# Optimization experiments

Hardware: AMD Instinct MI355X
Metric: run time of the kernel (lower is better)

The kernel has to match this reference:

```python
import jax, jax.numpy as jnp
import numpy as np

DIM = 1024
HEADS = 16
DIM_HEAD = 64
INNER = HEADS * DIM_HEAD  # 1024
SCALE = DIM_HEAD ** -0.5


def setup_inputs() -> dict:
    key = jax.random.key(0)
    ks = jax.random.split(key, 5)
    B, N = 4, 2048
    x = jax.random.normal(ks[0], (B, N, DIM), dtype=jnp.float32)
    # torch Linear weights are [out, in]; store transposed [in, out] for x @ W
    s = 1.0 / np.sqrt(DIM)
    Wq = jax.random.uniform(ks[1], (DIM, INNER), minval=-s, maxval=s, dtype=jnp.float32)
    Wkv = jax.random.uniform(ks[2], (DIM, 2 * INNER), minval=-s, maxval=s, dtype=jnp.float32)
    so = 1.0 / np.sqrt(INNER)
    Wo = jax.random.uniform(ks[3], (INNER, DIM), minval=-so, maxval=so, dtype=jnp.float32)
    bo = jax.random.uniform(ks[4], (DIM,), minval=-so, maxval=so, dtype=jnp.float32)
    return {"x": x, "Wq": Wq, "Wkv": Wkv, "Wo": Wo, "bo": bo}


def reference(x, Wq, Wkv, Wo, bo):
    B, N, _ = x.shape
    q = x @ Wq                      # [B, N, INNER]
    kv = x @ Wkv                    # [B, N, 2*INNER]
    k, v = jnp.split(kv, 2, axis=-1)

    def split_heads(t):
        return t.reshape(B, N, HEADS, DIM_HEAD).transpose(0, 2, 1, 3)  # [B,H,N,D]

    q, k, v = split_heads(q) * SCALE, split_heads(k), split_heads(v)
    sim = jnp.einsum('bhid,bhjd->bhij', q, k)  # [B,H,N,N]
    mask_value = -jnp.finfo(sim.dtype).max
    # causal: mask strictly-upper triangle (triu with offset j-i+1 = 1)
    causal_mask = jnp.triu(jnp.ones((N, N), dtype=bool), k=1)
    sim = jnp.where(causal_mask[None, None, :, :], mask_value, sim)
    attn = jax.nn.softmax(sim, axis=-1)
    out = jnp.einsum('bhij,bhjd->bhid', attn, v)            # [B,H,N,D]
    out = out.transpose(0, 2, 1, 3).reshape(B, N, INNER)    # [B,N,INNER]
    return out @ Wo + bo
```

## Files before the change

kernel.cpp:

```cpp
#include <hip/hip_runtime.h>

typedef unsigned short u16;
typedef __bf16 bf16x8 __attribute__((ext_vector_type(8)));
typedef float floatx4 __attribute__((ext_vector_type(4)));
typedef unsigned as1_u32 __attribute__((address_space(1)));
typedef unsigned as3_u32 __attribute__((address_space(3)));

__device__ inline u16 f2bf(float f) {
    unsigned int u = __builtin_bit_cast(unsigned int, f);
    u += 0x7fffu + ((u >> 16) & 1u);
    return (u16)(u >> 16);
}
__device__ inline floatx4 mfma16(bf16x8 a, bf16x8 b, floatx4 c) {
    return __builtin_amdgcn_mfma_f32_16x16x32_bf16(a, b, c, 0, 0, 0);
}
__device__ inline void gld16(const u16* g, u16* l) {
    __builtin_amdgcn_global_load_lds((const as1_u32*)g, (as3_u32*)l, 16, 0, 0);
}
__device__ inline unsigned permpack(float lo, float hi) {
    return __builtin_amdgcn_perm(__builtin_bit_cast(unsigned, hi),
                                 __builtin_bit_cast(unsigned, lo), 0x07060302u);
}

#define NSEQ 2048
#define DIM  1024
#define HEADS 16
#define DHEAD 64
#define QSCALE 0.18033688f
#define CSHIFT 4.328085f

__device__ inline void transpose_tile(const float* __restrict__ src,
                                      u16* __restrict__ dst, int ncols,
                                      int n0, int k0, int t) {
    __shared__ u16 tile[64][72];
    #pragma unroll
    for (int rr = 0; rr < 4; rr++) {
        const int k = (t >> 4) + rr * 16;
        const int n = (t & 15) * 4;
        float4 v = *(const float4*)&src[(size_t)(k0 + k) * ncols + n0 + n];
        tile[n + 0][k] = f2bf(v.x); tile[n + 1][k] = f2bf(v.y);
        tile[n + 2][k] = f2bf(v.z); tile[n + 3][k] = f2bf(v.w);
    }
    __syncthreads();
    #pragma unroll
    for (int ww = 0; ww < 2; ww++) {
        const int idx = t + ww * 256;
        const int n = idx >> 3, g = idx & 7;
        u16 tmp[8] __attribute__((aligned(16)));
        #pragma unroll
        for (int i = 0; i < 8; i++) tmp[i] = tile[n][g * 8 + i];
        *(uint4*)&dst[(size_t)(n0 + n) * 1024 + k0 + g * 8] = *(const uint4*)tmp;
    }
}

__global__ __launch_bounds__(256) void prep_fused(
    const float* __restrict__ x,  u16* __restrict__ xb,
    const float* __restrict__ Wq, const float* __restrict__ Wkv,
    u16* __restrict__ Wt)
{
    const int bid = blockIdx.x;
    const int t = threadIdx.x;
    if (bid < 4096) {
        const size_t i = ((size_t)bid * 256 + t) * 8;
        float4 a = *(const float4*)&x[i];
        float4 b = *(const float4*)&x[i + 4];
        u16 o[8] __attribute__((aligned(16)));
        o[0] = f2bf(a.x); o[1] = f2bf(a.y); o[2] = f2bf(a.z); o[3] = f2bf(a.w);
        o[4] = f2bf(b.x); o[5] = f2bf(b.y); o[6] = f2bf(b.z); o[7] = f2bf(b.w);
        *(uint4*)&xb[i] = *(const uint4*)o;
    } else if (bid < 4352) {
        const int v = bid - 4096;
        transpose_tile(Wq, Wt, 1024, (v & 15) * 64, (v >> 4) * 64, t);
    } else {
        const int v = bid - 4352;
        transpose_tile(Wkv, Wt + (size_t)1024 * 1024, 2048, (v & 31) * 64, (v >> 5) * 64, t);
    }
}

__global__ __launch_bounds__(256) void transpose_conv(const float* __restrict__ src,
                                                      u16* __restrict__ dst, int ncols) {
    transpose_tile(src, dst, ncols, blockIdx.x * 64, blockIdx.y * 64, threadIdx.x);
}

__global__ __launch_bounds__(256) void qkv_gemm_v6(
    const u16* __restrict__ xb, const u16* __restrict__ Wt,
    u16* __restrict__ q_ws, u16* __restrict__ k_ws, u16* __restrict__ v_ws)
{
    __shared__ u16 As[2][2][128 * 32];
    __shared__ u16 Bs[2][2][128 * 32];

    const int n0 = blockIdx.x * 128;
    const int m0 = blockIdx.y * 128;
    const int t = threadIdx.x, lane = t & 63, w = t >> 6;
    const int wr = w >> 1, wc = w & 1;
    const int quad = lane >> 4, l16 = lane & 15;
    const int lrow = lane >> 2;
    const int lk = (((lane & 3) ^ ((lane >> 3) & 3)) * 8);
    const int rsw = ((l16 >> 1) & 3);

    floatx4 acc[4][4];
    #pragma unroll
    for (int i = 0; i < 4; i++)
        #pragma unroll
        for (int j = 0; j < 4; j++) acc[i][j] = floatx4{0.f, 0.f, 0.f, 0.f};

#define STAGE_V6(kt, buf) do {                                             \
    const size_t k0s = (size_t)(kt) * 64;                                  \
    _Pragma("unroll")                                                      \
    for (int hh = 0; hh < 2; hh++) {                                       \
        const int row = w * 32 + hh * 16;                                  \
        const size_t ga = (size_t)(m0 + row + lrow) * DIM + k0s + lk;      \
        const size_t gb = (size_t)(n0 + row + lrow) * DIM + k0s + lk;      \
        gld16(&xb[ga],      &As[buf][0][row * 32]);                        \
        gld16(&xb[ga + 32], &As[buf][1][row * 32]);                        \
        gld16(&Wt[gb],      &Bs[buf][0][row * 32]);                        \
        gld16(&Wt[gb + 32], &Bs[buf][1][row * 32]);                        \
    }                                                                      \
} while (0)

    STAGE_V6(0, 0);
    STAGE_V6(1, 1);

    for (int kt = 0; kt < 16; kt++) {
        const int cur = kt & 1;
        if (kt < 15) asm volatile("s_waitcnt vmcnt(8)" ::: "memory");
        else         asm volatile("s_waitcnt vmcnt(0)" ::: "memory");
        __builtin_amdgcn_s_barrier();
        __builtin_amdgcn_sched_barrier(0);

        #pragma unroll
        for (int ks = 0; ks < 2; ks++) {
            const u16* al = &As[cur][ks][0];
            const u16* bl = &Bs[cur][ks][0];
            bf16x8 af[4], bf[4];
            #pragma unroll
            for (int i = 0; i < 4; i++)
                af[i] = *(const bf16x8*)&al[(wr * 64 + i * 16 + l16) * 32
                                            + ((quad ^ rsw) * 8)];
            #pragma unroll
            for (int j = 0; j < 4; j++)
                bf[j] = *(const bf16x8*)&bl[(wc * 64 + j * 16 + l16) * 32
                                            + ((quad ^ rsw) * 8)];
            __builtin_amdgcn_s_setprio(1);
            #pragma unroll
            for (int i = 0; i < 4; i++)
                #pragma unroll
                for (int j = 0; j < 4; j++)
                    acc[i][j] = mfma16(af[i], bf[j], acc[i][j]);
            __builtin_amdgcn_s_setprio(0);
        }

        __builtin_amdgcn_sched_barrier(0);
        __builtin_amdgcn_s_barrier();
        __builtin_amdgcn_sched_barrier(0);
        if (kt < 14) STAGE_V6(kt + 2, cur);
    }
#undef STAGE_V6

    const int seg = n0 >> 10;
    #pragma unroll
    for (int j = 0; j < 4; j++) {
        const int n  = n0 + wc * 64 + j * 16 + l16;
        const int nn = n & 1023;
        const int h  = nn >> 6, d = nn & 63;
        #pragma unroll
        for (int i = 0; i < 4; i++) {
            const int mb = m0 + wr * 64 + i * 16 + quad * 4;
            const int b = mb >> 11, ib = mb & (NSEQ - 1);
            if (seg == 0) {
                #pragma unroll
                for (int r = 0; r < 4; r++)
                    q_ws[(((size_t)(b * HEADS + h)) * NSEQ + ib + r) * DHEAD + d] =
                        f2bf(acc[i][j][r] * QSCALE);
            } else if (seg == 1) {
                #pragma unroll
                for (int r = 0; r < 4; r++)
                    k_ws[(((size_t)(b * HEADS + h)) * NSEQ + ib + r) * DHEAD + d] =
                        f2bf(acc[i][j][r]);
            } else {
                u16 tmp[4] __attribute__((aligned(8)));
                #pragma unroll
                for (int r = 0; r < 4; r++) tmp[r] = f2bf(acc[i][j][r]);
                *(uint2*)&v_ws[(((size_t)(b * HEADS + h)) * DHEAD + d) * NSEQ + ib] =
                    *(const uint2*)tmp;
            }
        }
    }
}

__global__ __launch_bounds__(256) void attn_v8(
    const u16* __restrict__ q_ws, const u16* __restrict__ k_ws,
    const u16* __restrict__ v_ws, u16* __restrict__ attn_ws)
{
    __shared__ u16 kds[2][64 * 64];
    __shared__ u16 vds[2][64 * 64];
    __shared__ u16 p_lds[4 * 2048];

    const int bid = blockIdx.x;
    const int bh  = bid & 63;
    const int t16 = 15 - (bid >> 6);
    const int i0  = t16 * 128;
    const int b   = bh >> 4, h = bh & 15;

    const u16* qb = q_ws + (size_t)bh * NSEQ * DHEAD;
    const u16* kb = k_ws + (size_t)bh * NSEQ * DHEAD;
    const u16* vb = v_ws + (size_t)bh * DHEAD * NSEQ;

    const int t    = threadIdx.x;
    const int lane = t & 63, w = t >> 6;
    const int quad = lane >> 4, l16 = lane & 15;

    const int srow8 = lane >> 3;
    const int chunk = (lane & 7) ^ srow8;
    const int krow  = w * 16 + srow8;
    const size_t koff = (size_t)krow * DHEAD + chunk * 8;
    const size_t voff = (size_t)krow * NSEQ + chunk * 8;
    u16* klbase = (u16*)&kds[0][0] + w * 1024;
    u16* vlbase = (u16*)&vds[0][0] + w * 1024;
    const int sw = (l16 & 7);

    bf16x8 qf[2][2];
    #pragma unroll
    for (int rf = 0; rf < 2; rf++)
        #pragma unroll
        for (int dg = 0; dg < 2; dg++)
            qf[rf][dg] = *(const bf16x8*)&qb[(size_t)(i0 + rf * 64 + w * 16 + l16) * DHEAD
                                             + dg * 32 + quad * 8];

    floatx4 l4[2] = {floatx4{0.f,0.f,0.f,0.f}, floatx4{0.f,0.f,0.f,0.f}};
    floatx4 acc[2][4];
    #pragma unroll
    for (int rf = 0; rf < 2; rf++)
        #pragma unroll
        for (int dg = 0; dg < 4; dg++) acc[rf][dg] = floatx4{0.f, 0.f, 0.f, 0.f};

    const int jt_max = 2 * t16 + 1;

    gld16(&kb[koff],             klbase);
    gld16(&kb[koff + 8 * DHEAD], klbase + 512);
    gld16(&vb[voff],             vlbase);
    gld16(&vb[voff + 8 * NSEQ],  vlbase + 512);

    for (int jt = 0; jt <= jt_max; jt++) {
        const int cur = jt & 1;
        __syncthreads();

        if (jt < jt_max) {
            const size_t j64 = (size_t)(jt + 1) * 64;
            const int nb = (cur ^ 1) * 4096;
            gld16(&kb[j64 * DHEAD + koff],             klbase + nb);
            gld16(&kb[j64 * DHEAD + koff + 8 * DHEAD], klbase + nb + 512);
            gld16(&vb[j64 + voff],                     vlbase + nb);
            gld16(&vb[j64 + voff + 8 * NSEQ],          vlbase + nb + 512);
        }

        const u16* kl = &kds[cur][0];
        const u16* vl = &vds[cur][0];
        const int j0 = jt * 64;

        floatx4 s[2][4];
        #pragma unroll
        for (int rf = 0; rf < 2; rf++)
            #pragma unroll
            for (int g = 0; g < 4; g++)
                s[rf][g] = floatx4{-CSHIFT, -CSHIFT, -CSHIFT, -CSHIFT};
        __builtin_amdgcn_s_setprio(1);
        #pragma unroll
        for (int dg = 0; dg < 2; dg++)
            #pragma unroll
            for (int g = 0; g < 4; g++) {
                bf16x8 kf = *(const bf16x8*)&kl[(g * 16 + l16) * 64
                                                + (((dg * 4 + quad) ^ sw) * 8)];
                s[0][g] = mfma16(kf, qf[0][dg], s[0][g]);
                s[1][g] = mfma16(kf, qf[1][dg], s[1][g]);
            }
        __builtin_amdgcn_s_setprio(0);

        #pragma unroll
        for (int rf = 0; rf < 2; rf++) {
            const int imin = i0 + rf * 64 + w * 16;
            if (j0 + 63 > imin) {
                const int i = imin + l16;
                #pragma unroll
                for (int g = 0; g < 4; g++) {
                    const int jb = j0 + g * 16 + quad * 4;
                    #pragma unroll
                    for (int r = 0; r < 4; r++)
                        if (jb + r > i) s[rf][g][r] = -1e30f;
                }
            }
        }

        #pragma unroll
        for (int rf = 0; rf < 2; rf++) {
            #pragma unroll
            for (int g = 0; g < 4; g++) {
                #pragma unroll
                for (int r = 0; r < 4; r++)
                    s[rf][g][r] = __builtin_amdgcn_exp2f(s[rf][g][r]);
                l4[rf] += s[rf][g];
                uint2 pk;
                pk.x = permpack(s[rf][g][0], s[rf][g][1]);
                pk.y = permpack(s[rf][g][2], s[rf][g][3]);
                const int c = 2 * g + (quad >> 1);
                *(uint2*)&p_lds[w * 2048 + rf * 1024 + (c >> 2) * 512 + (c & 3) * 128
                                + l16 * 8 + (quad & 1) * 4] = pk;
            }
        }
        asm volatile("s_waitcnt lgkmcnt(0)" ::: "memory");

        __builtin_amdgcn_s_setprio(1);
        #pragma unroll
        for (int jg = 0; jg < 2; jg++) {
            bf16x8 pf0 = *(const bf16x8*)&p_lds[w * 2048 + jg * 512 + quad * 128 + l16 * 8];
            bf16x8 pf1 = *(const bf16x8*)&p_lds[w * 2048 + 1024 + jg * 512 + quad * 128 + l16 * 8];
            #pragma unroll
            for (int dg = 0; dg < 4; dg++) {
                bf16x8 vf = *(const bf16x8*)&vl[(dg * 16 + l16) * 64
                                                + (((jg * 4 + quad) ^ sw) * 8)];
                acc[0][dg] = mfma16(pf0, vf, acc[0][dg]);
                acc[1][dg] = mfma16(pf1, vf, acc[1][dg]);
            }
        }
        __builtin_amdgcn_s_setprio(0);
    }

    #pragma unroll
    for (int rf = 0; rf < 2; rf++) {
        float l_ln = (l4[rf][0] + l4[rf][1]) + (l4[rf][2] + l4[rf][3]);
        l_ln += __shfl_xor(l_ln, 16);
        l_ln += __shfl_xor(l_ln, 32);
        float linv[4];
        #pragma unroll
        for (int r = 0; r < 4; r++)
            linv[r] = 1.0f / __shfl(l_ln, quad * 4 + r);
        #pragma unroll
        for (int dg = 0; dg < 4; dg++)
            #pragma unroll
            for (int r = 0; r < 4; r++) {
                const float o = acc[rf][dg][r] * linv[r];
                const int i = i0 + rf * 64 + w * 16 + quad * 4 + r;
                attn_ws[(((size_t)(b * NSEQ + i)) * HEADS + h) * DHEAD + dg * 16 + l16] =
                    f2bf(o);
            }
    }
}

__global__ __launch_bounds__(256) void out_gemm_v6(
    const u16* __restrict__ attn, const u16* __restrict__ Wot,
    const float* __restrict__ bo, float* __restrict__ out)
{
    __shared__ u16 As[2][2][128 * 32];
    __shared__ u16 Bs[2][2][128 * 32];

    const int n0 = blockIdx.x * 128;
    const int m0 = blockIdx.y * 128;
    const int t = threadIdx.x, lane = t & 63, w = t >> 6;
    const int wr = w >> 1, wc = w & 1;
    const int quad = lane >> 4, l16 = lane & 15;
    const int lrow = lane >> 2;
    const int lk = (((lane & 3) ^ ((lane >> 3) & 3)) * 8);
    const int rsw = ((l16 >> 1) & 3);

    floatx4 acc[4][4];
    #pragma unroll
    for (int i = 0; i < 4; i++)
        #pragma unroll
        for (int j = 0; j < 4; j++) acc[i][j] = floatx4{0.f, 0.f, 0.f, 0.f};

#define STAGE_O6(kt, buf) do {                                             \
    const size_t k0s = (size_t)(kt) * 64;                                  \
    _Pragma("unroll")                                                      \
    for (int hh = 0; hh < 2; hh++) {                                       \
        const int row = w * 32 + hh * 16;                                  \
        const size_t ga = (size_t)(m0 + row + lrow) * DIM + k0s + lk;      \
        const size_t gb = (size_t)(n0 + row + lrow) * DIM + k0s + lk;      \
        gld16(&attn[ga],      &As[buf][0][row * 32]);                      \
        gld16(&attn[ga + 32], &As[buf][1][row * 32]);                      \
        gld16(&Wot[gb],       &Bs[buf][0][row * 32]);                      \
        gld16(&Wot[gb + 32],  &Bs[buf][1][row * 32]);                      \
    }                                                                      \
} while (0)

    STAGE_O6(0, 0);
    STAGE_O6(1, 1);

    for (int kt = 0; kt < 16; kt++) {
        const int cur = kt & 1;
        if (kt < 15) asm volatile("s_waitcnt vmcnt(8)" ::: "memory");
        else         asm volatile("s_waitcnt vmcnt(0)" ::: "memory");
        __builtin_amdgcn_s_barrier();
        __builtin_amdgcn_sched_barrier(0);

        #pragma unroll
        for (int ks = 0; ks < 2; ks++) {
            const u16* al = &As[cur][ks][0];
            const u16* bl = &Bs[cur][ks][0];
            bf16x8 af[4], bf[4];
            #pragma unroll
            for (int i = 0; i < 4; i++)
                af[i] = *(const bf16x8*)&al[(wr * 64 + i * 16 + l16) * 32
                                            + ((quad ^ rsw) * 8)];
            #pragma unroll
            for (int j = 0; j < 4; j++)
                bf[j] = *(const bf16x8*)&bl[(wc * 64 + j * 16 + l16) * 32
                                            + ((quad ^ rsw) * 8)];
            __builtin_amdgcn_s_setprio(1);
            #pragma unroll
            for (int i = 0; i < 4; i++)
                #pragma unroll
                for (int j = 0; j < 4; j++)
                    acc[i][j] = mfma16(af[i], bf[j], acc[i][j]);
            __builtin_amdgcn_s_setprio(0);
        }

        __builtin_amdgcn_sched_barrier(0);
        __builtin_amdgcn_s_barrier();
        __builtin_amdgcn_sched_barrier(0);
        if (kt < 14) STAGE_O6(kt + 2, cur);
    }
#undef STAGE_O6

    #pragma unroll
    for (int j = 0; j < 4; j++) {
        const int n = n0 + wc * 64 + j * 16 + l16;
        const float bias = bo[n];
        #pragma unroll
        for (int i = 0; i < 4; i++) {
            #pragma unroll
            for (int r = 0; r < 4; r++) {
                const int m = m0 + wr * 64 + i * 16 + quad * 4 + r;
                out[(size_t)m * DIM + n] = acc[i][j][r] + bias;
            }
        }
    }
}

extern "C" void kernel_launch(void* const* d_in, const int* in_sizes, int n_in,
                              void* d_out, int out_size, void* d_ws, size_t ws_size,
                              hipStream_t stream) {
    const float* x   = (const float*)d_in[0];
    const float* Wq  = (const float*)d_in[1];
    const float* Wkv = (const float*)d_in[2];
    const float* Wo  = (const float*)d_in[3];
    const float* bo  = (const float*)d_in[4];

    u16* q_ws = (u16*)d_out;
    u16* xb   = (u16*)d_out + (size_t)8388608;

    u16* ws   = (u16*)d_ws;
    u16* k_ws = ws;
    u16* v_ws = ws + (size_t)8388608;
    u16* a_ws = ws + (size_t)16777216;
    u16* Wt   = a_ws;
    u16* Wot  = k_ws;

    prep_fused<<<4864, 256, 0, stream>>>(x, xb, Wq, Wkv, Wt);
    qkv_gemm_v6<<<dim3(24, 64), 256, 0, stream>>>(xb, Wt, q_ws, k_ws, v_ws);
    attn_v8<<<dim3(1024), 256, 0, stream>>>(q_ws, k_ws, v_ws, a_ws);
    transpose_conv<<<dim3(16, 16), 256, 0, stream>>>(Wo, Wot, 1024);
    out_gemm_v6<<<dim3(8, 64), 256, 0, stream>>>(a_ws, Wot, bo, (float*)d_out);
}
```

Baseline: 249.8 us.

## Pair causal query tiles per block to balance attention work

Each attention block now processes two 64-row query tiles, one near the start and one near the end of the sequence, so every block performs the same number of key tiles. This removes causal load imbalance across blocks. In exchange each K/V tile loaded into LDS is reused by only 64 query rows instead of 128, roughly doubling K/V load traffic and barriers per unit of compute.

```diff
diff --git a/kernel.cpp b/kernel.cpp
--- a/kernel.cpp
+++ b/kernel.cpp
@@ -188,18 +188,17 @@
     }
 }
 
-__global__ __launch_bounds__(256) void attn_v8(
+__global__ __launch_bounds__(256) void attn_v9(
     const u16* __restrict__ q_ws, const u16* __restrict__ k_ws,
     const u16* __restrict__ v_ws, u16* __restrict__ attn_ws)
 {
     __shared__ u16 kds[2][64 * 64];
     __shared__ u16 vds[2][64 * 64];
-    __shared__ u16 p_lds[4 * 2048];
+    __shared__ u16 p_lds[4 * 1024];
 
     const int bid = blockIdx.x;
     const int bh  = bid & 63;
-    const int t16 = 15 - (bid >> 6);
-    const int i0  = t16 * 128;
+    const int pr  = bid >> 6;
     const int b   = bh >> 4, h = bh & 15;
 
     const u16* qb = q_ws + (size_t)bh * NSEQ * DHEAD;
@@ -219,115 +218,102 @@
     u16* vlbase = (u16*)&vds[0][0] + w * 1024;
     const int sw = (l16 & 7);
 
-    bf16x8 qf[2][2];
-    #pragma unroll
-    for (int rf = 0; rf < 2; rf++)
+    for (int seg = 0; seg < 2; seg++) {
+        const int tq = seg ? pr : (31 - pr);
+        const int i0 = tq * 64;
+        const int jt_max = tq;
+
+        bf16x8 qf[2];
         #pragma unroll
         for (int dg = 0; dg < 2; dg++)
-            qf[rf][dg] = *(const bf16x8*)&qb[(size_t)(i0 + rf * 64 + w * 16 + l16) * DHEAD
-                                             + dg * 32 + quad * 8];
-
-    floatx4 l4[2] = {floatx4{0.f,0.f,0.f,0.f}, floatx4{0.f,0.f,0.f,0.f}};
-    floatx4 acc[2][4];
-    #pragma unroll
-    for (int rf = 0; rf < 2; rf++)
-        #pragma unroll
-        for (int dg = 0; dg < 4; dg++) acc[rf][dg] = floatx4{0.f, 0.f, 0.f, 0.f};
-
-    const int jt_max = 2 * t16 + 1;
-
-    gld16(&kb[koff],             klbase);
-    gld16(&kb[koff + 8 * DHEAD], klbase + 512);
-    gld16(&vb[voff],             vlbase);
-    gld16(&vb[voff + 8 * NSEQ],  vlbase + 512);
-
-    for (int jt = 0; jt <= jt_max; jt++) {
-        const int cur = jt & 1;
+            qf[dg] = *(const bf16x8*)&qb[(size_t)(i0 + w * 16 + l16) * DHEAD
+                                         + dg * 32 + quad * 8];
+
+        floatx4 l4 = floatx4{0.f, 0.f, 0.f, 0.f};
+        floatx4 acc[4];
+        #pragma unroll
+        for (int dg = 0; dg < 4; dg++) acc[dg] = floatx4{0.f, 0.f, 0.f, 0.f};
+
         __syncthreads();
-
-        if (jt < jt_max) {
-            const size_t j64 = (size_t)(jt + 1) * 64;
-            const int nb = (cur ^ 1) * 4096;
-            gld16(&kb[j64 * DHEAD + koff],             klbase + nb);
-            gld16(&kb[j64 * DHEAD + koff + 8 * DHEAD], klbase + nb + 512);
-            gld16(&vb[j64 + voff],                     vlbase + nb);
-            gld16(&vb[j64 + voff + 8 * NSEQ],          vlbase + nb + 512);
-        }
-
-        const u16* kl = &kds[cur][0];
-        const u16* vl = &vds[cur][0];
-        const int j0 = jt * 64;
-
-        floatx4 s[2][4];
-        #pragma unroll
-        for (int rf = 0; rf < 2; rf++)
+        gld16(&kb[koff],             klbase);
+        gld16(&kb[koff + 8 * DHEAD], klbase + 512);
+        gld16(&vb[voff],             vlbase);
+        gld16(&vb[voff + 8 * NSEQ],  vlbase + 512);
+
+        for (int jt = 0; jt <= jt_max; jt++) {
+            const int cur = jt & 1;
+            __syncthreads();
+
+            if (jt < jt_max) {
+                const size_t j64 = (size_t)(jt + 1) * 64;
+                const int nb = (cur ^ 1) * 4096;
+                gld16(&kb[j64 * DHEAD + koff],             klbase + nb);
+                gld16(&kb[j64 * DHEAD + koff + 8 * DHEAD], klbase + nb + 512);
+                gld16(&vb[j64 + voff],                     vlbase + nb);
+                gld16(&vb[j64 + voff + 8 * NSEQ],          vlbase + nb + 512);
+            }
+
+            const u16* kl = &kds[cur][0];
+            const u16* vl = &vds[cur][0];
+            const int j0 = jt * 64;
+
+            floatx4 s[4];
             #pragma unroll
             for (int g = 0; g < 4; g++)
-                s[rf][g] = floatx4{-CSHIFT, -CSHIFT, -CSHIFT, -CSHIFT};
-        __builtin_amdgcn_s_setprio(1);
-        #pragma unroll
-        for (int dg = 0; dg < 2; dg++)
-            #pragma unroll
-            for (int g = 0; g < 4; g++) {
-                bf16x8 kf = *(const bf16x8*)&kl[(g * 16 + l16) * 64
-                                                + (((dg * 4 + quad) ^ sw) * 8)];
-                s[0][g] = mfma16(kf, qf[0][dg], s[0][g]);
-                s[1][g] = mfma16(kf, qf[1][dg], s[1][g]);
-            }
-        __builtin_amdgcn_s_setprio(0);
-
-        #pragma unroll
-        for (int rf = 0; rf < 2; rf++) {
-            const int imin = i0 + rf * 64 + w * 16;
-            if (j0 + 63 > imin) {
-                const int i = imin + l16;
+                s[g] = floatx4{-CSHIFT, -CSHIFT, -CSHIFT, -CSHIFT};
+            __builtin_amdgcn_s_setprio(1);
+            #pragma unroll
+            for (int dg = 0; dg < 2; dg++)
+                #pragma unroll
+                for (int g = 0; g < 4; g++) {
+                    bf16x8 kf = *(const bf16x8*)&kl[(g * 16 + l16) * 64
+                                                    + (((dg * 4 + quad) ^ sw) * 8)];
+                    s[g] = mfma16(kf, qf[dg], s[g]);
+                }
+            __builtin_amdgcn_s_setprio(0);
+
+            if (j0 + 63 > i0 + w * 16) {
+                const int i = i0 + w * 16 + l16;
                 #pragma unroll
                 for (int g = 0; g < 4; g++) {
                     const int jb = j0 + g * 16 + quad * 4;
                     #pragma unroll
                     for (int r = 0; r < 4; r++)
-                        if (jb + r > i) s[rf][g][r] = -1e30f;
+                        if (jb + r > i) s[g][r] = -1e30f;
                 }
             }
+
+            #pragma unroll
+            for (int g = 0; g < 4; g++) {
+                #pragma unroll
+                for (int r = 0; r < 4; r++)
+                    s[g][r] = __builtin_amdgcn_exp2f(s[g][r]);
+                l4 += s[g];
+                uint2 pk;
+                pk.x = permpack(s[g][0], s[g][1]);
+                pk.y = permpack(s[g][2], s[g][3]);
+                const int c = 2 * g + (quad >> 1);
+                *(uint2*)&p_lds[w * 1024 + (c >> 2) * 512 + (c & 3) * 128
+                                + l16 * 8 + (quad & 1) * 4] = pk;
+            }
+            asm volatile("s_waitcnt lgkmcnt(0)" ::: "memory");
+
+            __builtin_amdgcn_s_setprio(1);
+            #pragma unroll
+            for (int jg = 0; jg < 2; jg++) {
+                bf16x8 pf = *(const bf16x8*)&p_lds[w * 1024 + jg * 512
+                                                   + quad * 128 + l16 * 8];
+                #pragma unroll
+                for (int dg = 0; dg < 4; dg++) {
+                    bf16x8 vf = *(const bf16x8*)&vl[(dg * 16 + l16) * 64
+                                                    + (((jg * 4 + quad) ^ sw) * 8)];
+                    acc[dg] = mfma16(pf, vf, acc[dg]);
+                }
+            }
+            __builtin_amdgcn_s_setprio(0);
         }
 
-        #pragma unroll
-        for (int rf = 0; rf < 2; rf++) {
-            #pragma unroll
-            for (int g = 0; g < 4; g++) {
-                #pragma unroll
-                for (int r = 0; r < 4; r++)
-                    s[rf][g][r] = __builtin_amdgcn_exp2f(s[rf][g][r]);
-                l4[rf] += s[rf][g];
-                uint2 pk;
-                pk.x = permpack(s[rf][g][0], s[rf][g][1]);
-                pk.y = permpack(s[rf][g][2], s[rf][g][3]);
-                const int c = 2 * g + (quad >> 1);
-                *(uint2*)&p_lds[w * 2048 + rf * 1024 + (c >> 2) * 512 + (c & 3) * 128
-                                + l16 * 8 + (quad & 1) * 4] = pk;
-            }
-        }
-        asm volatile("s_waitcnt lgkmcnt(0)" ::: "memory");
-
-        __builtin_amdgcn_s_setprio(1);
-        #pragma unroll
-        for (int jg = 0; jg < 2; jg++) {
-            bf16x8 pf0 = *(const bf16x8*)&p_lds[w * 2048 + jg * 512 + quad * 128 + l16 * 8];
-            bf16x8 pf1 = *(const bf16x8*)&p_lds[w * 2048 + 1024 + jg * 512 + quad * 128 + l16 * 8];
-            #pragma unroll
-            for (int dg = 0; dg < 4; dg++) {
-                bf16x8 vf = *(const bf16x8*)&vl[(dg * 16 + l16) * 64
-                                                + (((jg * 4 + quad) ^ sw) * 8)];
-                acc[0][dg] = mfma16(pf0, vf, acc[0][dg]);
-                acc[1][dg] = mfma16(pf1, vf, acc[1][dg]);
-            }
-        }
-        __builtin_amdgcn_s_setprio(0);
-    }
-
-    #pragma unroll
-    for (int rf = 0; rf < 2; rf++) {
-        float l_ln = (l4[rf][0] + l4[rf][1]) + (l4[rf][2] + l4[rf][3]);
+        float l_ln = (l4[0] + l4[1]) + (l4[2] + l4[3]);
         l_ln += __shfl_xor(l_ln, 16);
         l_ln += __shfl_xor(l_ln, 32);
         float linv[4];
@@ -338,8 +324,8 @@
         for (int dg = 0; dg < 4; dg++)
             #pragma unroll
             for (int r = 0; r < 4; r++) {
-                const float o = acc[rf][dg][r] * linv[r];
-                const int i = i0 + rf * 64 + w * 16 + quad * 4 + r;
+                const float o = acc[dg][r] * linv[r];
+                const int i = i0 + w * 16 + quad * 4 + r;
                 attn_ws[(((size_t)(b * NSEQ + i)) * HEADS + h) * DHEAD + dg * 16 + l16] =
                     f2bf(o);
             }
@@ -457,7 +443,7 @@
 
     prep_fused<<<4864, 256, 0, stream>>>(x, xb, Wq, Wkv, Wt);
     qkv_gemm_v6<<<dim3(24, 64), 256, 0, stream>>>(xb, Wt, q_ws, k_ws, v_ws);
-    attn_v8<<<dim3(1024), 256, 0, stream>>>(q_ws, k_ws, v_ws, a_ws);
+    attn_v9<<<dim3(1024), 256, 0, stream>>>(q_ws, k_ws, v_ws, a_ws);
     transpose_conv<<<dim3(16, 16), 256, 0, stream>>>(Wo, Wot, 1024);
     out_gemm_v6<<<dim3(8, 64), 256, 0, stream>>>(a_ws, Wot, bo, (float*)d_out);
 }
```

After: 243.2 us. 2.7% less time.
